# Optimization experiments

Hardware: AMD Instinct MI355X
Metric: run time of the kernel (lower is better)

## Reference

```python
import jax, jax.numpy as jnp
import numpy as np

B, N, D, OBS, H = 1024, 128, 1024, 256, 256  # batch, num_samples, act_dim, obs_dim, hidden
K = 1
SIGMA = 0.05


def perturbed_topk(x, noise):
    # x: [B, D] softmax probs; noise: [B, N, D]
    perturbed = x[:, None, :] + noise * SIGMA            # [B, N, D]
    idx = jax.lax.top_k(perturbed, K)[1]                 # [B, N, K]
    idx = jnp.sort(idx, axis=-1)
    onehot = jax.nn.one_hot(idx, D, dtype=jnp.float32)   # [B, N, K, D]
    return onehot.mean(axis=1)                           # [B, K, D]


def setup_inputs() -> dict:
    key = jax.random.key(0)
    ks = jax.random.split(key, 12)
    rn = lambda k, s, sc: jax.random.normal(k, s, jnp.float32) * sc
    return {
        "obs": rn(ks[0], (B, OBS), 1.0),
        "noise": rn(ks[1], (B, N, D), 1.0),
        "W1": rn(ks[2], (OBS, H), 1.0 / np.sqrt(OBS)),
        "b1": jnp.zeros((H,), jnp.float32),
        "W2": rn(ks[3], (H, H), 1.0 / np.sqrt(H)),
        "b2": jnp.zeros((H,), jnp.float32),
        "W3": rn(ks[4], (H, D), 1.0 / np.sqrt(H)),
        "b3": jnp.zeros((D,), jnp.float32),
        "Wv1": rn(ks[5], (OBS + 1, H), 1.0 / np.sqrt(OBS + 1)),
        "bv1": jnp.zeros((H,), jnp.float32),
        "Wv2": rn(ks[6], (H, 1), 1.0 / np.sqrt(H)),
        "bv2": jnp.zeros((1,), jnp.float32),
    }


def reference(obs, noise, W1, b1, W2, b2, W3, b3, Wv1, bv1, Wv2, bv2):
    # policy MLP (tanh hidden, identity output) then softmax
    h = jnp.tanh(obs @ W1 + b1)
    h = jnp.tanh(h @ W2 + b2)
    probs = jax.nn.softmax(h @ W3 + b3, axis=-1)         # [B, D]
    indicators = perturbed_topk(probs, noise)            # [B, K, D]
    index_table = jnp.arange(D, dtype=jnp.float32)
    approx_argmax = jnp.sum(indicators * index_table)    # scalar (sum over ALL dims, as in source)
    obs_act = jnp.concatenate(
        [obs, jnp.broadcast_to(approx_argmax, (obs.shape[0], 1))], axis=1
    )                                                     # [B, OBS+1]
    v = jnp.tanh(obs_act @ Wv1 + bv1)
    Q = v @ Wv2 + bv2                                     # [B, 1]
    return Q
```

## Files before the change

kernel.cpp:

```cpp
#include <hip/hip_runtime.h>
#include <math.h>

#define SIGMA 0.05f

__global__ __launch_bounds__(256) void fc_tanh_kernel(
    const float* __restrict__ in, const float* __restrict__ W,
    const float* __restrict__ bias, float* __restrict__ out,
    int* acc_zero)
{
    __shared__ float s[256];
    const int b = blockIdx.x, j = threadIdx.x;
    s[j] = in[b * 256 + j];
    __syncthreads();
    float acc = bias[j];
#pragma unroll 8
    for (int k = 0; k < 256; ++k)
        acc = fmaf(s[k], W[k * 256 + j], acc);
    out[b * 256 + j] = tanhf(acc);
    if (acc_zero != nullptr && b == 0 && j == 0) *acc_zero = 0;
}

__global__ __launch_bounds__(256) void fc3_kernel(
    const float* __restrict__ h2, const float* __restrict__ W3,
    const float* __restrict__ b3, float* __restrict__ logits)
{
    __shared__ float s[8 * 256];
    const int tid = threadIdx.x;
    const int col = blockIdx.x * 256 + tid;
    const int row0 = blockIdx.y * 8;
#pragma unroll
    for (int r = 0; r < 8; ++r)
        s[r * 256 + tid] = h2[(row0 + r) * 256 + tid];
    __syncthreads();
    float acc[8];
    const float bb = b3[col];
#pragma unroll
    for (int r = 0; r < 8; ++r) acc[r] = bb;
    for (int k = 0; k < 256; ++k) {
        const float w = W3[(size_t)k * 1024 + col];
#pragma unroll
        for (int r = 0; r < 8; ++r)
            acc[r] = fmaf(s[r * 256 + k], w, acc[r]);
    }
#pragma unroll
    for (int r = 0; r < 8; ++r)
        logits[(size_t)(row0 + r) * 1024 + col] = acc[r];
}

__global__ __launch_bounds__(256) void softmax_kernel(float* __restrict__ logits)
{
    __shared__ float red[4];
    const int b = blockIdx.x, tid = threadIdx.x;
    const int lane = tid & 63, wave = tid >> 6;
    float* row = logits + (size_t)b * 1024;
    float4 v = *(const float4*)(row + tid * 4);

    float m = fmaxf(fmaxf(v.x, v.y), fmaxf(v.z, v.w));
#pragma unroll
    for (int off = 1; off < 64; off <<= 1) m = fmaxf(m, __shfl_xor(m, off));
    if (lane == 0) red[wave] = m;
    __syncthreads();
    const float M = fmaxf(fmaxf(red[0], red[1]), fmaxf(red[2], red[3]));

    float4 e;
    e.x = expf(v.x - M); e.y = expf(v.y - M);
    e.z = expf(v.z - M); e.w = expf(v.w - M);
    float ssum = e.x + e.y + e.z + e.w;
#pragma unroll
    for (int off = 1; off < 64; off <<= 1) ssum += __shfl_xor(ssum, off);
    __syncthreads();
    if (lane == 0) red[wave] = ssum;
    __syncthreads();
    const float inv = 1.0f / (red[0] + red[1] + red[2] + red[3]);
    e.x *= inv; e.y *= inv; e.z *= inv; e.w *= inv;
    *(float4*)(row + tid * 4) = e;
}

#define NSPLIT 4
__global__ __launch_bounds__(256) void argmax_kernel(
    const float* __restrict__ probs, const float* __restrict__ noise,
    int* __restrict__ acc)
{
    __shared__ float ps[1024];
    __shared__ int wsum[4];
    const int b = blockIdx.x / NSPLIT;
    const int part = blockIdx.x % NSPLIT;
    const int tid = threadIdx.x;
    const int lane = tid & 63, wave = tid >> 6;

    for (int i = tid; i < 1024; i += 256)
        ps[i] = probs[(size_t)b * 1024 + i];
    __syncthreads();

    const int nper = 128 / NSPLIT;
    int mysum = 0;
    for (int ni = wave; ni < nper; ni += 4) {
        const int n = part * nper + ni;
        const float* __restrict__ np_ = noise + ((size_t)b * 128 + n) * 1024;

        const float4 n0 = *(const float4*)(np_ + (size_t)(lane        ) * 4);
        const float4 n1 = *(const float4*)(np_ + (size_t)(lane +  64) * 4);
        const float4 n2 = *(const float4*)(np_ + (size_t)(lane + 128) * 4);
        const float4 n3 = *(const float4*)(np_ + (size_t)(lane + 192) * 4);
        const float4 p0 = *(const float4*)(ps + (lane        ) * 4);
        const float4 p1 = *(const float4*)(ps + (lane +  64) * 4);
        const float4 p2 = *(const float4*)(ps + (lane + 128) * 4);
        const float4 p3 = *(const float4*)(ps + (lane + 192) * 4);

        float best = -1e30f; int bidx = 0;
#define CHK(val, d) { float _v = (val); if (_v > best) { best = _v; bidx = (d); } }
        int d0 = lane * 4;
        CHK(fmaf(n0.x, SIGMA, p0.x), d0 + 0); CHK(fmaf(n0.y, SIGMA, p0.y), d0 + 1);
        CHK(fmaf(n0.z, SIGMA, p0.z), d0 + 2); CHK(fmaf(n0.w, SIGMA, p0.w), d0 + 3);
        d0 = (lane + 64) * 4;
        CHK(fmaf(n1.x, SIGMA, p1.x), d0 + 0); CHK(fmaf(n1.y, SIGMA, p1.y), d0 + 1);
        CHK(fmaf(n1.z, SIGMA, p1.z), d0 + 2); CHK(fmaf(n1.w, SIGMA, p1.w), d0 + 3);
        d0 = (lane + 128) * 4;
        CHK(fmaf(n2.x, SIGMA, p2.x), d0 + 0); CHK(fmaf(n2.y, SIGMA, p2.y), d0 + 1);
        CHK(fmaf(n2.z, SIGMA, p2.z), d0 + 2); CHK(fmaf(n2.w, SIGMA, p2.w), d0 + 3);
        d0 = (lane + 192) * 4;
        CHK(fmaf(n3.x, SIGMA, p3.x), d0 + 0); CHK(fmaf(n3.y, SIGMA, p3.y), d0 + 1);
        CHK(fmaf(n3.z, SIGMA, p3.z), d0 + 2); CHK(fmaf(n3.w, SIGMA, p3.w), d0 + 3);
#undef CHK

#pragma unroll
        for (int off = 1; off < 64; off <<= 1) {
            const float ov = __shfl_xor(best, off);
            const int   oi = __shfl_xor(bidx, off);
            if (ov > best || (ov == best && oi < bidx)) { best = ov; bidx = oi; }
        }
        mysum += bidx;
    }
    if (lane == 0) wsum[wave] = mysum;
    __syncthreads();
    if (tid == 0)
        atomicAdd(acc, wsum[0] + wsum[1] + wsum[2] + wsum[3]);
}

__global__ __launch_bounds__(256) void value_kernel(
    const float* __restrict__ obs, const float* __restrict__ Wv1,
    const float* __restrict__ bv1, const float* __restrict__ Wv2,
    const float* __restrict__ bv2, const int* __restrict__ acc,
    float* __restrict__ Q)
{
    __shared__ float s[256];
    __shared__ float red[4];
    const int b = blockIdx.x, j = threadIdx.x;
    const int lane = j & 63, wave = j >> 6;
    s[j] = obs[b * 256 + j];
    __syncthreads();
    const float c = (float)(*acc) * (1.0f / 128.0f);
    float a = bv1[j] + c * Wv1[256 * 256 + j];
#pragma unroll 8
    for (int k = 0; k < 256; ++k)
        a = fmaf(s[k], Wv1[k * 256 + j], a);
    float v = tanhf(a) * Wv2[j];
#pragma unroll
    for (int off = 1; off < 64; off <<= 1) v += __shfl_xor(v, off);
    if (lane == 0) red[wave] = v;
    __syncthreads();
    if (j == 0) Q[b] = red[0] + red[1] + red[2] + red[3] + bv2[0];
}

extern "C" void kernel_launch(void* const* d_in, const int* in_sizes, int n_in,
                              void* d_out, int out_size, void* d_ws, size_t ws_size,
                              hipStream_t stream)
{
    const float* obs   = (const float*)d_in[0];
    const float* noise = (const float*)d_in[1];
    const float* W1    = (const float*)d_in[2];
    const float* b1    = (const float*)d_in[3];
    const float* W2    = (const float*)d_in[4];
    const float* b2    = (const float*)d_in[5];
    const float* W3    = (const float*)d_in[6];
    const float* b3    = (const float*)d_in[7];
    const float* Wv1   = (const float*)d_in[8];
    const float* bv1   = (const float*)d_in[9];
    const float* Wv2   = (const float*)d_in[10];
    const float* bv2   = (const float*)d_in[11];
    float* Q = (float*)d_out;

    float* ws     = (float*)d_ws;
    float* h1     = ws;
    float* h2     = h1 + 1024 * 256;
    float* logits = h2 + 1024 * 256;
    int*   acc    = (int*)(logits + 1024 * 1024);

    fc_tanh_kernel<<<1024, 256, 0, stream>>>(obs, W1, b1, h1, acc);
    fc_tanh_kernel<<<1024, 256, 0, stream>>>(h1, W2, b2, h2, nullptr);
    fc3_kernel<<<dim3(4, 128), 256, 0, stream>>>(h2, W3, b3, logits);
    softmax_kernel<<<1024, 256, 0, stream>>>(logits);
    argmax_kernel<<<1024 * NSPLIT, 256, 0, stream>>>(logits, noise, acc);
    value_kernel<<<1024, 256, 0, stream>>>(obs, Wv1, bv1, Wv2, bv2, acc, Q);
}
```

Measured before the change: 774.6 us.

## Fuse policy MLP layers and softmax into one kernel; unroll argmax noise loop

Merges the two hidden tanh layers, the output layer and the softmax into a single 1024-thread kernel that handles 4 batch rows per block. Activations stay in shared memory, so the h1/h2/logits round-trips through global memory and three launches go away. The argmax kernel now hoists the probability loads out of the loop and handles two noise samples per iteration, giving more loads in flight. The cost is only 256 blocks for the fused MLP, fewer than before, and W3 is reused across 4 rows instead of 8, so the output-layer matmul may fill the GPU less well.

```diff
diff --git a/kernel.cpp b/kernel.cpp
--- a/kernel.cpp
+++ b/kernel.cpp
@@ -3,80 +3,123 @@
 
 #define SIGMA 0.05f
 
-__global__ __launch_bounds__(256) void fc_tanh_kernel(
-    const float* __restrict__ in, const float* __restrict__ W,
-    const float* __restrict__ bias, float* __restrict__ out,
-    int* acc_zero)
-{
-    __shared__ float s[256];
-    const int b = blockIdx.x, j = threadIdx.x;
-    s[j] = in[b * 256 + j];
-    __syncthreads();
-    float acc = bias[j];
+__global__ __launch_bounds__(1024) void mlp_kernel(
+    const float* __restrict__ obs,
+    const float* __restrict__ W1, const float* __restrict__ b1,
+    const float* __restrict__ W2, const float* __restrict__ b2,
+    const float* __restrict__ W3, const float* __restrict__ b3,
+    float* __restrict__ probs, int* acc_zero)
+{
+    __shared__ float sobs[4 * 256];
+    __shared__ float sh1[4 * 256];
+    __shared__ float sh2[4 * 256];
+    __shared__ float red[4][17];
+    const int tid = threadIdx.x;
+    const int r = tid >> 8, j = tid & 255;
+    const int b0 = blockIdx.x * 4;
+    const int lane = tid & 63, wave = tid >> 6;
+
+    sobs[tid] = obs[(b0 + r) * 256 + j];
+    if (blockIdx.x == 0 && tid == 0) *acc_zero = 0;
+    __syncthreads();
+
+    float a = b1[j];
 #pragma unroll 8
     for (int k = 0; k < 256; ++k)
-        acc = fmaf(s[k], W[k * 256 + j], acc);
-    out[b * 256 + j] = tanhf(acc);
-    if (acc_zero != nullptr && b == 0 && j == 0) *acc_zero = 0;
-}
-
-__global__ __launch_bounds__(256) void fc3_kernel(
-    const float* __restrict__ h2, const float* __restrict__ W3,
-    const float* __restrict__ b3, float* __restrict__ logits)
-{
-    __shared__ float s[8 * 256];
-    const int tid = threadIdx.x;
-    const int col = blockIdx.x * 256 + tid;
-    const int row0 = blockIdx.y * 8;
-#pragma unroll
-    for (int r = 0; r < 8; ++r)
-        s[r * 256 + tid] = h2[(row0 + r) * 256 + tid];
-    __syncthreads();
-    float acc[8];
+        a = fmaf(sobs[r * 256 + k], W1[k * 256 + j], a);
+    sh1[tid] = tanhf(a);
+    __syncthreads();
+
+    a = b2[j];
+#pragma unroll 8
+    for (int k = 0; k < 256; ++k)
+        a = fmaf(sh1[r * 256 + k], W2[k * 256 + j], a);
+    sh2[tid] = tanhf(a);
+    __syncthreads();
+
+    const int col = tid;
+    float acc4[4];
     const float bb = b3[col];
-#pragma unroll
-    for (int r = 0; r < 8; ++r) acc[r] = bb;
+    acc4[0] = acc4[1] = acc4[2] = acc4[3] = bb;
+#pragma unroll 4
     for (int k = 0; k < 256; ++k) {
-        const float w = W3[(size_t)k * 1024 + col];
-#pragma unroll
-        for (int r = 0; r < 8; ++r)
-            acc[r] = fmaf(s[r * 256 + k], w, acc[r]);
-    }
-#pragma unroll
-    for (int r = 0; r < 8; ++r)
-        logits[(size_t)(row0 + r) * 1024 + col] = acc[r];
-}
-
-__global__ __launch_bounds__(256) void softmax_kernel(float* __restrict__ logits)
-{
-    __shared__ float red[4];
-    const int b = blockIdx.x, tid = threadIdx.x;
-    const int lane = tid & 63, wave = tid >> 6;
-    float* row = logits + (size_t)b * 1024;
-    float4 v = *(const float4*)(row + tid * 4);
-
-    float m = fmaxf(fmaxf(v.x, v.y), fmaxf(v.z, v.w));
-#pragma unroll
-    for (int off = 1; off < 64; off <<= 1) m = fmaxf(m, __shfl_xor(m, off));
-    if (lane == 0) red[wave] = m;
-    __syncthreads();
-    const float M = fmaxf(fmaxf(red[0], red[1]), fmaxf(red[2], red[3]));
-
-    float4 e;
-    e.x = expf(v.x - M); e.y = expf(v.y - M);
-    e.z = expf(v.z - M); e.w = expf(v.w - M);
-    float ssum = e.x + e.y + e.z + e.w;
-#pragma unroll
-    for (int off = 1; off < 64; off <<= 1) ssum += __shfl_xor(ssum, off);
-    __syncthreads();
-    if (lane == 0) red[wave] = ssum;
-    __syncthreads();
-    const float inv = 1.0f / (red[0] + red[1] + red[2] + red[3]);
-    e.x *= inv; e.y *= inv; e.z *= inv; e.w *= inv;
-    *(float4*)(row + tid * 4) = e;
+        const float w = W3[k * 1024 + col];
+        acc4[0] = fmaf(sh2[0 * 256 + k], w, acc4[0]);
+        acc4[1] = fmaf(sh2[1 * 256 + k], w, acc4[1]);
+        acc4[2] = fmaf(sh2[2 * 256 + k], w, acc4[2]);
+        acc4[3] = fmaf(sh2[3 * 256 + k], w, acc4[3]);
+    }
+
+    float M[4];
+#pragma unroll
+    for (int rr = 0; rr < 4; ++rr) {
+        float m = acc4[rr];
+#pragma unroll
+        for (int off = 1; off < 64; off <<= 1) m = fmaxf(m, __shfl_xor(m, off));
+        if (lane == 0) red[rr][wave] = m;
+    }
+    __syncthreads();
+#pragma unroll
+    for (int rr = 0; rr < 4; ++rr) {
+        float m = red[rr][0];
+#pragma unroll
+        for (int wv = 1; wv < 16; ++wv) m = fmaxf(m, red[rr][wv]);
+        M[rr] = m;
+    }
+    __syncthreads();
+#pragma unroll
+    for (int rr = 0; rr < 4; ++rr) {
+        float e = expf(acc4[rr] - M[rr]);
+        acc4[rr] = e;
+#pragma unroll
+        for (int off = 1; off < 64; off <<= 1) e += __shfl_xor(e, off);
+        if (lane == 0) red[rr][wave] = e;
+    }
+    __syncthreads();
+#pragma unroll
+    for (int rr = 0; rr < 4; ++rr) {
+        float s = 0.f;
+#pragma unroll
+        for (int wv = 0; wv < 16; ++wv) s += red[rr][wv];
+        probs[(size_t)(b0 + rr) * 1024 + col] = acc4[rr] / s;
+    }
 }
 
 #define NSPLIT 4
+
+__device__ __forceinline__ void scan16(
+    const float4 n0, const float4 n1, const float4 n2, const float4 n3,
+    const float4 p0, const float4 p1, const float4 p2, const float4 p3,
+    int lane, float& best, int& bidx)
+{
+    best = -1e30f; bidx = 0;
+#define CHK(val, d) { float _v = (val); if (_v > best) { best = _v; bidx = (d); } }
+    int d0 = lane * 4;
+    CHK(fmaf(n0.x, SIGMA, p0.x), d0 + 0); CHK(fmaf(n0.y, SIGMA, p0.y), d0 + 1);
+    CHK(fmaf(n0.z, SIGMA, p0.z), d0 + 2); CHK(fmaf(n0.w, SIGMA, p0.w), d0 + 3);
+    d0 = (lane + 64) * 4;
+    CHK(fmaf(n1.x, SIGMA, p1.x), d0 + 0); CHK(fmaf(n1.y, SIGMA, p1.y), d0 + 1);
+    CHK(fmaf(n1.z, SIGMA, p1.z), d0 + 2); CHK(fmaf(n1.w, SIGMA, p1.w), d0 + 3);
+    d0 = (lane + 128) * 4;
+    CHK(fmaf(n2.x, SIGMA, p2.x), d0 + 0); CHK(fmaf(n2.y, SIGMA, p2.y), d0 + 1);
+    CHK(fmaf(n2.z, SIGMA, p2.z), d0 + 2); CHK(fmaf(n2.w, SIGMA, p2.w), d0 + 3);
+    d0 = (lane + 192) * 4;
+    CHK(fmaf(n3.x, SIGMA, p3.x), d0 + 0); CHK(fmaf(n3.y, SIGMA, p3.y), d0 + 1);
+    CHK(fmaf(n3.z, SIGMA, p3.z), d0 + 2); CHK(fmaf(n3.w, SIGMA, p3.w), d0 + 3);
+#undef CHK
+}
+
+__device__ __forceinline__ int wave_argmax(float best, int bidx)
+{
+#pragma unroll
+    for (int off = 1; off < 64; off <<= 1) {
+        const float ov = __shfl_xor(best, off);
+        const int   oi = __shfl_xor(bidx, off);
+        if (ov > best || (ov == best && oi < bidx)) { best = ov; bidx = oi; }
+    }
+    return bidx;
+}
+
 __global__ __launch_bounds__(256) void argmax_kernel(
     const float* __restrict__ probs, const float* __restrict__ noise,
     int* __restrict__ acc)
@@ -92,44 +135,31 @@
         ps[i] = probs[(size_t)b * 1024 + i];
     __syncthreads();
 
-    const int nper = 128 / NSPLIT;
+    const float4 p0 = *(const float4*)(ps + (lane       ) * 4);
+    const float4 p1 = *(const float4*)(ps + (lane +  64) * 4);
+    const float4 p2 = *(const float4*)(ps + (lane + 128) * 4);
+    const float4 p3 = *(const float4*)(ps + (lane + 192) * 4);
+
+    const int nbase = part * 32 + wave * 8;
     int mysum = 0;
-    for (int ni = wave; ni < nper; ni += 4) {
-        const int n = part * nper + ni;
-        const float* __restrict__ np_ = noise + ((size_t)b * 128 + n) * 1024;
-
-        const float4 n0 = *(const float4*)(np_ + (size_t)(lane        ) * 4);
-        const float4 n1 = *(const float4*)(np_ + (size_t)(lane +  64) * 4);
-        const float4 n2 = *(const float4*)(np_ + (size_t)(lane + 128) * 4);
-        const float4 n3 = *(const float4*)(np_ + (size_t)(lane + 192) * 4);
-        const float4 p0 = *(const float4*)(ps + (lane        ) * 4);
-        const float4 p1 = *(const float4*)(ps + (lane +  64) * 4);
-        const float4 p2 = *(const float4*)(ps + (lane + 128) * 4);
-        const float4 p3 = *(const float4*)(ps + (lane + 192) * 4);
-
-        float best = -1e30f; int bidx = 0;
-#define CHK(val, d) { float _v = (val); if (_v > best) { best = _v; bidx = (d); } }
-        int d0 = lane * 4;
-        CHK(fmaf(n0.x, SIGMA, p0.x), d0 + 0); CHK(fmaf(n0.y, SIGMA, p0.y), d0 + 1);
-        CHK(fmaf(n0.z, SIGMA, p0.z), d0 + 2); CHK(fmaf(n0.w, SIGMA, p0.w), d0 + 3);
-        d0 = (lane + 64) * 4;
-        CHK(fmaf(n1.x, SIGMA, p1.x), d0 + 0); CHK(fmaf(n1.y, SIGMA, p1.y), d0 + 1);
-        CHK(fmaf(n1.z, SIGMA, p1.z), d0 + 2); CHK(fmaf(n1.w, SIGMA, p1.w), d0 + 3);
-        d0 = (lane + 128) * 4;
-        CHK(fmaf(n2.x, SIGMA, p2.x), d0 + 0); CHK(fmaf(n2.y, SIGMA, p2.y), d0 + 1);
-        CHK(fmaf(n2.z, SIGMA, p2.z), d0 + 2); CHK(fmaf(n2.w, SIGMA, p2.w), d0 + 3);
-        d0 = (lane + 192) * 4;
-        CHK(fmaf(n3.x, SIGMA, p3.x), d0 + 0); CHK(fmaf(n3.y, SIGMA, p3.y), d0 + 1);
-        CHK(fmaf(n3.z, SIGMA, p3.z), d0 + 2); CHK(fmaf(n3.w, SIGMA, p3.w), d0 + 3);
-#undef CHK
-
-#pragma unroll
-        for (int off = 1; off < 64; off <<= 1) {
-            const float ov = __shfl_xor(best, off);
-            const int   oi = __shfl_xor(bidx, off);
-            if (ov > best || (ov == best && oi < bidx)) { best = ov; bidx = oi; }
-        }
-        mysum += bidx;
+    for (int i = 0; i < 8; i += 2) {
+        const float* __restrict__ npa = noise + ((size_t)b * 128 + nbase + i    ) * 1024;
+        const float* __restrict__ npb = noise + ((size_t)b * 128 + nbase + i + 1) * 1024;
+
+        const float4 a0 = *(const float4*)(npa + (size_t)(lane       ) * 4);
+        const float4 a1 = *(const float4*)(npa + (size_t)(lane +  64) * 4);
+        const float4 a2 = *(const float4*)(npa + (size_t)(lane + 128) * 4);
+        const float4 a3 = *(const float4*)(npa + (size_t)(lane + 192) * 4);
+        const float4 c0 = *(const float4*)(npb + (size_t)(lane       ) * 4);
+        const float4 c1 = *(const float4*)(npb + (size_t)(lane +  64) * 4);
+        const float4 c2 = *(const float4*)(npb + (size_t)(lane + 128) * 4);
+        const float4 c3 = *(const float4*)(npb + (size_t)(lane + 192) * 4);
+
+        float bestA, bestB; int idxA, idxB;
+        scan16(a0, a1, a2, a3, p0, p1, p2, p3, lane, bestA, idxA);
+        scan16(c0, c1, c2, c3, p0, p1, p2, p3, lane, bestB, idxB);
+        mysum += wave_argmax(bestA, idxA);
+        mysum += wave_argmax(bestB, idxB);
     }
     if (lane == 0) wsum[wave] = mysum;
     __syncthreads();
@@ -180,16 +210,10 @@
     const float* bv2   = (const float*)d_in[11];
     float* Q = (float*)d_out;
 
-    float* ws     = (float*)d_ws;
-    float* h1     = ws;
-    float* h2     = h1 + 1024 * 256;
-    float* logits = h2 + 1024 * 256;
-    int*   acc    = (int*)(logits + 1024 * 1024);
-
-    fc_tanh_kernel<<<1024, 256, 0, stream>>>(obs, W1, b1, h1, acc);
-    fc_tanh_kernel<<<1024, 256, 0, stream>>>(h1, W2, b2, h2, nullptr);
-    fc3_kernel<<<dim3(4, 128), 256, 0, stream>>>(h2, W3, b3, logits);
-    softmax_kernel<<<1024, 256, 0, stream>>>(logits);
-    argmax_kernel<<<1024 * NSPLIT, 256, 0, stream>>>(logits, noise, acc);
+    float* probs = (float*)d_ws;
+    int*   acc   = (int*)(probs + 1024 * 1024);
+
+    mlp_kernel<<<256, 1024, 0, stream>>>(obs, W1, b1, W2, b2, W3, b3, probs, acc);
+    argmax_kernel<<<1024 * NSPLIT, 256, 0, stream>>>(probs, noise, acc);
     value_kernel<<<1024, 256, 0, stream>>>(obs, Wv1, bv1, Wv2, bv2, acc, Q);
 }
```

Result: no change. 778.3 us (+0.5%).
